# Performance work log

Measured on AMD Instinct MI355X. Metric: run time of the kernel, lower is better.

The kernel has to match this reference:

```python
import jax, jax.numpy as jnp
import numpy as np

N_NODES = 50000
N_EDGES = 800000
F_IN = 256
HID = 128
HEADS = 4
F_OUT = 64
NEG_SLOPE = 0.2


def setup_inputs() -> dict:
    key = jax.random.key(0)
    ks = jax.random.split(key, 12)
    x = jax.random.normal(ks[0], (N_NODES, F_IN), dtype=jnp.float32)
    edge_index = jax.random.randint(ks[1], (2, N_EDGES), 0, N_NODES, dtype=jnp.int64)
    s = 0.05
    return {
        "x": x,
        "edge_index": edge_index,
        "W1": jax.random.normal(ks[2], (F_IN, HEADS * HID), dtype=jnp.float32) * s,
        "a_src1": jax.random.normal(ks[3], (HEADS, HID), dtype=jnp.float32) * s,
        "a_dst1": jax.random.normal(ks[4], (HEADS, HID), dtype=jnp.float32) * s,
        "b1": jnp.zeros((HEADS * HID,), dtype=jnp.float32),
        "W2": jax.random.normal(ks[5], (HEADS * HID, F_OUT), dtype=jnp.float32) * s,
        "a_src2": jax.random.normal(ks[6], (1, F_OUT), dtype=jnp.float32) * s,
        "a_dst2": jax.random.normal(ks[7], (1, F_OUT), dtype=jnp.float32) * s,
        "b2": jnp.zeros((F_OUT,), dtype=jnp.float32),
    }


def _add_self_loops(edge_index, n):
    loop = jnp.arange(n, dtype=edge_index.dtype)
    return jnp.concatenate([edge_index, jnp.stack([loop, loop])], axis=1)


def _gat_conv(x, edge_index, W, a_src, a_dst, bias, heads, out_ch):
    # PyG GATConv: h = x @ W reshaped to [N, H, C]
    n = x.shape[0]
    h = (x @ W).reshape(n, heads, out_ch)
    # per-node attention logits [N, H]
    al_src = jnp.einsum('nhc,hc->nh', h, a_src)
    al_dst = jnp.einsum('nhc,hc->nh', h, a_dst)
    src, dst = edge_index[0], edge_index[1]
    e = jax.nn.leaky_relu(al_src[src] + al_dst[dst], NEG_SLOPE)  # [E, H]
    # softmax over incoming edges per destination node (segment softmax)
    e_max = jax.ops.segment_max(e, dst, num_segments=n)
    e_exp = jnp.exp(e - e_max[dst])
    denom = jax.ops.segment_sum(e_exp, dst, num_segments=n)
    alpha = e_exp / (denom[dst] + 1e-16)  # [E, H]
    msg = h[src] * alpha[:, :, None]  # [E, H, C]
    out = jax.ops.segment_sum(msg, dst, num_segments=n)  # [N, H, C]
    return out.reshape(n, heads * out_ch) + bias


def reference(x, edge_index, W1, a_src1, a_dst1, b1, W2, a_src2, a_dst2, b2):
    # Dropout layers are identity in eval mode.
    ei = _add_self_loops(edge_index, x.shape[0])
    h = jax.nn.elu(_gat_conv(x, ei, W1, a_src1, a_dst1, b1, HEADS, HID))
    out = _gat_conv(h, ei, W2, a_src2, a_dst2, b2, 1, F_OUT)
    return out
```

## Files before the change

kernel.cpp:

```cpp
#include <hip/hip_runtime.h>
#include <math.h>

#define N_NODES 50000
#define N_EDGES 800000
#define E_TOT   850000
#define F_IN    256
#define F1      512
#define HID     128
#define HEADS   4
#define F_OUT   64

typedef __attribute__((ext_vector_type(8))) short short8;
typedef __attribute__((ext_vector_type(4))) float f32x4;
typedef unsigned short ushort_t;
typedef unsigned int uint_t;

__device__ __forceinline__ float lrelu(float x){ return x > 0.f ? x : 0.2f*x; }
__device__ __forceinline__ float elu(float x){ return x > 0.f ? x : expm1f(x); }

__device__ __forceinline__ ushort_t f2b(float f){
  uint_t u = __builtin_bit_cast(uint_t, f);
  u += 0x7fffu + ((u >> 16) & 1u);
  return (ushort_t)(u >> 16);
}
__device__ __forceinline__ float blo(uint_t u){ return __builtin_bit_cast(float, u << 16); }
__device__ __forceinline__ float bhi(uint_t u){ return __builtin_bit_cast(float, u & 0xffff0000u); }
__device__ __forceinline__ float b2f(ushort_t s){ return __builtin_bit_cast(float, (uint_t)s << 16); }

__global__ void hist_kernel(const int* __restrict__ ei, int* __restrict__ deg){
  int e = blockIdx.x*blockDim.x + threadIdx.x;
  if (e >= E_TOT) return;
  int dst = (e < N_EDGES) ? ei[N_EDGES + e] : (e - N_EDGES);
  atomicAdd(&deg[dst], 1);
}

__global__ __launch_bounds__(256) void scan1_kernel(const int* __restrict__ deg,
                                                    int* __restrict__ offs,
                                                    int* __restrict__ bsum){
  __shared__ int sd[256];
  const int tid = threadIdx.x;
  const int i = blockIdx.x*256 + tid;
  int v = (i < N_NODES) ? deg[i] : 0;
  sd[tid] = v; __syncthreads();
  #pragma unroll
  for (int off = 1; off < 256; off <<= 1){
    int t = (tid >= off) ? sd[tid - off] : 0;
    __syncthreads();
    sd[tid] += t;
    __syncthreads();
  }
  if (i < N_NODES) offs[i] = sd[tid] - v;
  if (tid == 255) bsum[blockIdx.x] = sd[255];
}

__global__ __launch_bounds__(256) void scan2_kernel(const int* __restrict__ bsum,
                                                    int* __restrict__ bbase, int nb){
  __shared__ int sd[256];
  const int tid = threadIdx.x;
  int v = (tid < nb) ? bsum[tid] : 0;
  sd[tid] = v; __syncthreads();
  #pragma unroll
  for (int off = 1; off < 256; off <<= 1){
    int t = (tid >= off) ? sd[tid - off] : 0;
    __syncthreads();
    sd[tid] += t;
    __syncthreads();
  }
  if (tid < nb) bbase[tid] = sd[tid] - v;
}

__global__ __launch_bounds__(256) void scan3_kernel(int* __restrict__ offs,
                                                    const int* __restrict__ bbase,
                                                    int* __restrict__ cur){
  const int i = blockIdx.x*256 + threadIdx.x;
  if (i < N_NODES){
    int o = offs[i] + bbase[blockIdx.x];
    offs[i] = o;
    cur[i] = o;
  }
  if (blockIdx.x == 0 && threadIdx.x == 0) offs[N_NODES] = E_TOT;
}

__global__ void scatter_kernel(const int* __restrict__ ei, int* __restrict__ cur,
                               int* __restrict__ ssrc){
  int e = blockIdx.x*blockDim.x + threadIdx.x;
  if (e >= E_TOT) return;
  int src, dst;
  if (e < N_EDGES){ src = ei[e]; dst = ei[N_EDGES + e]; }
  else            { src = e - N_EDGES; dst = src; }
  int pos = atomicAdd(&cur[dst], 1);
  ssrc[pos] = src;
}

__global__ __launch_bounds__(256) void cvt_x_kernel(const float* __restrict__ x,
                                                    ushort_t* __restrict__ xb){
  const int t = blockIdx.x*256 + threadIdx.x;
  const float4 a = ((const float4*)x)[t*2];
  const float4 b = ((const float4*)x)[t*2 + 1];
  uint4 o;
  o.x = (uint_t)f2b(a.x) | ((uint_t)f2b(a.y) << 16);
  o.y = (uint_t)f2b(a.z) | ((uint_t)f2b(a.w) << 16);
  o.z = (uint_t)f2b(b.x) | ((uint_t)f2b(b.y) << 16);
  o.w = (uint_t)f2b(b.z) | ((uint_t)f2b(b.w) << 16);
  ((uint4*)xb)[t] = o;
}

__global__ __launch_bounds__(256) void transpose_bf16_kernel(const float* __restrict__ W,
                                                             ushort_t* __restrict__ Wt,
                                                             int K, int N){
  __shared__ float tile[64][65];
  const int k0 = blockIdx.x*64, n0 = blockIdx.y*64;
  const int c = threadIdx.x & 63, r4 = threadIdx.x >> 6;
  for (int r = r4; r < 64; r += 4)
    tile[r][c] = W[(size_t)(k0 + r)*N + n0 + c];
  __syncthreads();
  for (int r = r4; r < 64; r += 4)
    Wt[(size_t)(n0 + r)*K + k0 + c] = f2b(tile[c][r]);
}

template<int K, int WR, int WC>
__global__ __launch_bounds__(256) void gemm_bf16(const ushort_t* __restrict__ A,
                                                 const ushort_t* __restrict__ Bt,
                                                 ushort_t* __restrict__ C,
                                                 int M, int N){
  constexpr int BM = WR*64, BN = WC*64, BKP = 40;
  __shared__ ushort_t As[BM*BKP];
  __shared__ ushort_t Bs[BN*BKP];
  const int tid = threadIdx.x;
  const int wave = tid >> 6, lane = tid & 63, quad = lane >> 4, l16 = lane & 15;
  const int wm = wave % WR, wn = wave / WR;
  const int m0 = blockIdx.x*BM, n0 = blockIdx.y*BN;
  f32x4 acc[4][4] = {};
  for (int k0 = 0; k0 < K; k0 += 32){
    #pragma unroll
    for (int s = tid; s < BM*4; s += 256){
      int r = s >> 2, c = s & 3;
      int gr = m0 + r; if (gr >= M) gr = M - 1;
      *(uint4*)(As + r*BKP + c*8) = *(const uint4*)(A + (size_t)gr*K + k0 + c*8);
    }
    #pragma unroll
    for (int s = tid; s < BN*4; s += 256){
      int r = s >> 2, c = s & 3;
      *(uint4*)(Bs + r*BKP + c*8) = *(const uint4*)(Bt + (size_t)(n0 + r)*K + k0 + c*8);
    }
    __syncthreads();
    short8 af[4], bfr[4];
    #pragma unroll
    for (int i = 0; i < 4; ++i)
      af[i] = *(const short8*)(As + (wm*64 + i*16 + l16)*BKP + quad*8);
    #pragma unroll
    for (int j = 0; j < 4; ++j)
      bfr[j] = *(const short8*)(Bs + (wn*64 + j*16 + l16)*BKP + quad*8);
    #pragma unroll
    for (int i = 0; i < 4; ++i)
      #pragma unroll
      for (int j = 0; j < 4; ++j)
        acc[i][j] = __builtin_amdgcn_mfma_f32_16x16x32_bf16(af[i], bfr[j], acc[i][j], 0, 0, 0);
    __syncthreads();
  }
  #pragma unroll
  for (int i = 0; i < 4; ++i){
    #pragma unroll
    for (int r = 0; r < 4; ++r){
      int row = m0 + wm*64 + i*16 + quad*4 + r;
      if (row < M){
        #pragma unroll
        for (int j = 0; j < 4; ++j){
          int col = n0 + wn*64 + j*16 + l16;
          C[(size_t)row*N + col] = f2b(acc[i][j][r]);
        }
      }
    }
  }
}

__global__ __launch_bounds__(128) void logits1_kernel(const ushort_t* __restrict__ h1b,
                                                      const float* __restrict__ a_src,
                                                      const float* __restrict__ a_dst,
                                                      float* __restrict__ als,
                                                      float* __restrict__ ald){
  const int n = blockIdx.x;
  const int tid = threadIdx.x;
  const int head = tid >> 5, p = tid & 31;
  const uint2 v = *(const uint2*)(h1b + (size_t)n*F1 + tid*4);
  float h0 = blo(v.x), h1 = bhi(v.x), h2 = blo(v.y), h3 = bhi(v.y);
  const float4 as = *(const float4*)(a_src + head*HID + p*4);
  const float4 ad = *(const float4*)(a_dst + head*HID + p*4);
  float ds = h0*as.x + h1*as.y + h2*as.z + h3*as.w;
  float dd = h0*ad.x + h1*ad.y + h2*ad.z + h3*ad.w;
  #pragma unroll
  for (int off = 16; off >= 1; off >>= 1){
    ds += __shfl_down(ds, off, 32);
    dd += __shfl_down(dd, off, 32);
  }
  if (p == 0){ als[n*4 + head] = ds; ald[n*4 + head] = dd; }
}

__global__ __launch_bounds__(256) void agg1_kernel(const ushort_t* __restrict__ h1b,
                                                   const float* __restrict__ als,
                                                   const float* __restrict__ ald1,
                                                   const float* __restrict__ b1,
                                                   const int* __restrict__ offs,
                                                   const int* __restrict__ ssrc,
                                                   ushort_t* __restrict__ hb){
  __shared__ int   shsrc[4][64];
  __shared__ float shal[4][64][4];
  const int wave = threadIdx.x >> 6, lane = threadIdx.x & 63;
  const int n = blockIdx.x*4 + wave;
  const int head = lane >> 4;
  const float4 ald = ((const float4*)ald1)[n];
  const int s0 = offs[n], s1 = offs[n+1];

  float d0 = 0.f, d1 = 0.f, d2 = 0.f, d3 = 0.f;
  for (int e = s0 + lane; e < s1; e += 64){
    const int sc = ssrc[e];
    const float4 as = ((const float4*)als)[sc];
    d0 += __expf(lrelu(as.x + ald.x));
    d1 += __expf(lrelu(as.y + ald.y));
    d2 += __expf(lrelu(as.z + ald.z));
    d3 += __expf(lrelu(as.w + ald.w));
  }
  #pragma unroll
  for (int off = 32; off >= 1; off >>= 1){
    d0 += __shfl_xor(d0, off);
    d1 += __shfl_xor(d1, off);
    d2 += __shfl_xor(d2, off);
    d3 += __shfl_xor(d3, off);
  }
  const float den = (head == 0) ? d0 : (head == 1) ? d1 : (head == 2) ? d2 : d3;
  const float rd = 1.0f / (den + 1e-16f);

  float acc[8] = {0.f,0.f,0.f,0.f,0.f,0.f,0.f,0.f};
  for (int ce = s0; ce < s1; ce += 64){
    const int idx = ce + lane;
    if (idx < s1){
      const int sc = ssrc[idx];
      const float4 as = ((const float4*)als)[sc];
      shsrc[wave][lane] = sc;
      float4 a4;
      a4.x = __expf(lrelu(as.x + ald.x));
      a4.y = __expf(lrelu(as.y + ald.y));
      a4.z = __expf(lrelu(as.z + ald.z));
      a4.w = __expf(lrelu(as.w + ald.w));
      *(float4*)&shal[wave][lane][0] = a4;
    }
    const int nE = min(64, s1 - ce);
    for (int k = 0; k < nE; ++k){
      const int scb = shsrc[wave][k];
      const float al = shal[wave][k][head] * rd;
      const uint4 hv = *(const uint4*)(h1b + (size_t)scb*F1 + lane*8);
      acc[0] = fmaf(blo(hv.x), al, acc[0]);
      acc[1] = fmaf(bhi(hv.x), al, acc[1]);
      acc[2] = fmaf(blo(hv.y), al, acc[2]);
      acc[3] = fmaf(bhi(hv.y), al, acc[3]);
      acc[4] = fmaf(blo(hv.z), al, acc[4]);
      acc[5] = fmaf(bhi(hv.z), al, acc[5]);
      acc[6] = fmaf(blo(hv.w), al, acc[6]);
      acc[7] = fmaf(bhi(hv.w), al, acc[7]);
    }
  }
  const float4 ba = *(const float4*)(b1 + lane*8);
  const float4 bb = *(const float4*)(b1 + lane*8 + 4);
  float o0 = elu(acc[0] + ba.x), o1 = elu(acc[1] + ba.y);
  float o2 = elu(acc[2] + ba.z), o3 = elu(acc[3] + ba.w);
  float o4 = elu(acc[4] + bb.x), o5 = elu(acc[5] + bb.y);
  float o6 = elu(acc[6] + bb.z), o7 = elu(acc[7] + bb.w);
  uint4 o;
  o.x = (uint_t)f2b(o0) | ((uint_t)f2b(o1) << 16);
  o.y = (uint_t)f2b(o2) | ((uint_t)f2b(o3) << 16);
  o.z = (uint_t)f2b(o4) | ((uint_t)f2b(o5) << 16);
  o.w = (uint_t)f2b(o6) | ((uint_t)f2b(o7) << 16);
  *(uint4*)(hb + (size_t)n*F1 + lane*8) = o;
}

__global__ __launch_bounds__(64) void logits2_kernel(const ushort_t* __restrict__ gb,
                                                     const float* __restrict__ a_src,
                                                     const float* __restrict__ a_dst,
                                                     float* __restrict__ als,
                                                     float* __restrict__ ald){
  const int n = blockIdx.x;
  const int tid = threadIdx.x;
  const float v = b2f(gb[(size_t)n*F_OUT + tid]);
  float ds = v * a_src[tid];
  float dd = v * a_dst[tid];
  #pragma unroll
  for (int off = 32; off >= 1; off >>= 1){
    ds += __shfl_xor(ds, off);
    dd += __shfl_xor(dd, off);
  }
  if (tid == 0){ als[n] = ds; ald[n] = dd; }
}

__global__ __launch_bounds__(256) void agg2_kernel(const ushort_t* __restrict__ gb,
                                                   const float* __restrict__ als,
                                                   const float* __restrict__ ald2,
                                                   const float* __restrict__ b2,
                                                   const int* __restrict__ offs,
                                                   const int* __restrict__ ssrc,
                                                   float* __restrict__ out){
  __shared__ int   shsrc[4][64];
  __shared__ float shal[4][64];
  const int wave = threadIdx.x >> 6, lane = threadIdx.x & 63;
  const int n = blockIdx.x*4 + wave;
  const float ald = ald2[n];
  const int s0 = offs[n], s1 = offs[n+1];

  float dsum = 0.f;
  for (int e = s0 + lane; e < s1; e += 64)
    dsum += __expf(lrelu(als[ssrc[e]] + ald));
  #pragma unroll
  for (int off = 32; off >= 1; off >>= 1)
    dsum += __shfl_xor(dsum, off);
  const float rd = 1.0f / (dsum + 1e-16f);

  float acc = 0.f;
  for (int ce = s0; ce < s1; ce += 64){
    const int idx = ce + lane;
    if (idx < s1){
      const int sc = ssrc[idx];
      shsrc[wave][lane] = sc;
      shal[wave][lane] = __expf(lrelu(als[sc] + ald)) * rd;
    }
    const int nE = min(64, s1 - ce);
    for (int k = 0; k < nE; ++k){
      const int scb = shsrc[wave][k];
      const float al = shal[wave][k];
      acc = fmaf(b2f(gb[(size_t)scb*F_OUT + lane]), al, acc);
    }
  }
  out[(size_t)n*F_OUT + lane] = acc + b2[lane];
}

extern "C" void kernel_launch(void* const* d_in, const int* in_sizes, int n_in,
                              void* d_out, int out_size, void* d_ws, size_t ws_size,
                              hipStream_t stream){
  const float* x      = (const float*)d_in[0];
  const int*   ei     = (const int*)  d_in[1];
  const float* W1     = (const float*)d_in[2];
  const float* a_src1 = (const float*)d_in[3];
  const float* a_dst1 = (const float*)d_in[4];
  const float* b1     = (const float*)d_in[5];
  const float* W2     = (const float*)d_in[6];
  const float* a_src2 = (const float*)d_in[7];
  const float* a_dst2 = (const float*)d_in[8];
  const float* b2     = (const float*)d_in[9];
  float* out = (float*)d_out;

  char* ws = (char*)d_ws;
  ushort_t* h1b  = (ushort_t*)(ws + 0UL);
  ushort_t* hb   = (ushort_t*)(ws + 51200000UL);
  ushort_t* xb   = (ushort_t*)(ws + 102400000UL);
  ushort_t* gb   = (ushort_t*)(ws + 128000000UL);
  ushort_t* W1t  = (ushort_t*)(ws + 134400000UL);
  ushort_t* W2t  = (ushort_t*)(ws + 134662144UL);
  float*    als1 = (float*)   (ws + 134727680UL);
  float*    ald1 = (float*)   (ws + 135527680UL);
  float*    als2 = (float*)   (ws + 136327680UL);
  float*    ald2 = (float*)   (ws + 136527680UL);
  int*      deg  = (int*)     (ws + 136727680UL);
  int*      offs = (int*)     (ws + 136927680UL);
  int*      bsum = (int*)     (ws + 137127744UL);
  int*      bbase= (int*)     (ws + 137128544UL);
  int*      cur  = (int*)     (ws + 137129600UL);
  int*      ssrc = (int*)     (ws + 137329600UL);

  hipMemsetAsync(deg, 0, 200000, stream);

  const int eb = (E_TOT + 255) / 256;
  const int nb = (N_NODES + 255) / 256;
  hist_kernel   <<<eb, 256, 0, stream>>>(ei, deg);
  scan1_kernel  <<<nb, 256, 0, stream>>>(deg, offs, bsum);
  scan2_kernel  <<<1, 256, 0, stream>>>(bsum, bbase, nb);
  scan3_kernel  <<<nb, 256, 0, stream>>>(offs, bbase, cur);
  scatter_kernel<<<eb, 256, 0, stream>>>(ei, cur, ssrc);

  cvt_x_kernel        <<<6250, 256, 0, stream>>>(x, xb);
  transpose_bf16_kernel<<<dim3(4, 8), 256, 0, stream>>>(W1, W1t, F_IN, F1);
  transpose_bf16_kernel<<<dim3(8, 1), 256, 0, stream>>>(W2, W2t, F1, F_OUT);

  gemm_bf16<F_IN, 2, 2><<<dim3(391, 4), 256, 0, stream>>>(xb, W1t, h1b, N_NODES, F1);
  logits1_kernel<<<N_NODES, 128, 0, stream>>>(h1b, a_src1, a_dst1, als1, ald1);
  agg1_kernel   <<<12500, 256, 0, stream>>>(h1b, als1, ald1, b1, offs, ssrc, hb);

  gemm_bf16<F1, 4, 1><<<dim3(196, 1), 256, 0, stream>>>(hb, W2t, gb, N_NODES, F_OUT);
  logits2_kernel<<<N_NODES, 64, 0, stream>>>(gb, a_src2, a_dst2, als2, ald2);
  agg2_kernel   <<<12500, 256, 0, stream>>>(gb, als2, ald2, b2, offs, ssrc, out);
}
```

Baseline: 476.8 us.

## Add single-pass fast path for low-degree nodes with software-prefetched gathers

For nodes with at most 64 incoming edges, the aggregation kernels now compute attention weights once into shared memory. They accumulate the unnormalized weighted sum and the softmax denominator in the same loop, then normalize at the end, removing the separate denominator pass over edges. The gather loop is unrolled by four and prefetches the next four source rows to hide memory latency. Padded slots use source 0 with zero weight, which adds a few redundant loads.

```diff
diff --git a/kernel.cpp b/kernel.cpp
--- a/kernel.cpp
+++ b/kernel.cpp
@@ -196,6 +196,16 @@
   if (p == 0){ als[n*4 + head] = ds; ald[n*4 + head] = dd; }
 }
 
+#define FMA8(hv, al) do{ \
+  acc[0] = fmaf(blo((hv).x), (al), acc[0]); \
+  acc[1] = fmaf(bhi((hv).x), (al), acc[1]); \
+  acc[2] = fmaf(blo((hv).y), (al), acc[2]); \
+  acc[3] = fmaf(bhi((hv).y), (al), acc[3]); \
+  acc[4] = fmaf(blo((hv).z), (al), acc[4]); \
+  acc[5] = fmaf(bhi((hv).z), (al), acc[5]); \
+  acc[6] = fmaf(blo((hv).w), (al), acc[6]); \
+  acc[7] = fmaf(bhi((hv).w), (al), acc[7]); }while(0)
+
 __global__ __launch_bounds__(256) void agg1_kernel(const ushort_t* __restrict__ h1b,
                                                    const float* __restrict__ als,
                                                    const float* __restrict__ ald1,
@@ -210,6 +220,73 @@
   const int head = lane >> 4;
   const float4 ald = ((const float4*)ald1)[n];
   const int s0 = offs[n], s1 = offs[n+1];
+  const int nE = s1 - s0;
+
+  float acc[8] = {0.f,0.f,0.f,0.f,0.f,0.f,0.f,0.f};
+
+  if (nE <= 64){
+    float4 a4 = {0.f,0.f,0.f,0.f};
+    int sc = 0;
+    if (lane < nE){
+      sc = ssrc[s0 + lane];
+      const float4 as = ((const float4*)als)[sc];
+      a4.x = __expf(lrelu(as.x + ald.x));
+      a4.y = __expf(lrelu(as.y + ald.y));
+      a4.z = __expf(lrelu(as.z + ald.z));
+      a4.w = __expf(lrelu(as.w + ald.w));
+    }
+    shsrc[wave][lane] = sc;
+    *(float4*)&shal[wave][lane][0] = a4;
+
+    const ushort_t* hbase = h1b + lane*8;
+    const int nE4 = (nE + 3) & ~3;
+    float dsum = 0.f;
+
+    uint4 h0  = *(const uint4*)(hbase + ((size_t)shsrc[wave][0] << 9));
+    uint4 h1v = *(const uint4*)(hbase + ((size_t)shsrc[wave][1] << 9));
+    uint4 h2v = *(const uint4*)(hbase + ((size_t)shsrc[wave][2] << 9));
+    uint4 h3v = *(const uint4*)(hbase + ((size_t)shsrc[wave][3] << 9));
+    float al0 = shal[wave][0][head];
+    float al1 = shal[wave][1][head];
+    float al2 = shal[wave][2][head];
+    float al3 = shal[wave][3][head];
+    for (int k = 0; k < nE4; k += 4){
+      uint4 p0 = h0, p1 = h1v, p2 = h2v, p3 = h3v;
+      float q0 = 0.f, q1 = 0.f, q2 = 0.f, q3 = 0.f;
+      if (k + 4 < nE4){
+        p0 = *(const uint4*)(hbase + ((size_t)shsrc[wave][k+4] << 9));
+        p1 = *(const uint4*)(hbase + ((size_t)shsrc[wave][k+5] << 9));
+        p2 = *(const uint4*)(hbase + ((size_t)shsrc[wave][k+6] << 9));
+        p3 = *(const uint4*)(hbase + ((size_t)shsrc[wave][k+7] << 9));
+        q0 = shal[wave][k+4][head];
+        q1 = shal[wave][k+5][head];
+        q2 = shal[wave][k+6][head];
+        q3 = shal[wave][k+7][head];
+      }
+      dsum += (al0 + al1) + (al2 + al3);
+      FMA8(h0,  al0);
+      FMA8(h1v, al1);
+      FMA8(h2v, al2);
+      FMA8(h3v, al3);
+      h0 = p0; h1v = p1; h2v = p2; h3v = p3;
+      al0 = q0; al1 = q1; al2 = q2; al3 = q3;
+    }
+
+    const float rd = 1.0f / (dsum + 1e-16f);
+    const float4 ba = *(const float4*)(b1 + lane*8);
+    const float4 bb = *(const float4*)(b1 + lane*8 + 4);
+    float o0 = elu(fmaf(acc[0], rd, ba.x)), o1 = elu(fmaf(acc[1], rd, ba.y));
+    float o2 = elu(fmaf(acc[2], rd, ba.z)), o3 = elu(fmaf(acc[3], rd, ba.w));
+    float o4 = elu(fmaf(acc[4], rd, bb.x)), o5 = elu(fmaf(acc[5], rd, bb.y));
+    float o6 = elu(fmaf(acc[6], rd, bb.z)), o7 = elu(fmaf(acc[7], rd, bb.w));
+    uint4 o;
+    o.x = (uint_t)f2b(o0) | ((uint_t)f2b(o1) << 16);
+    o.y = (uint_t)f2b(o2) | ((uint_t)f2b(o3) << 16);
+    o.z = (uint_t)f2b(o4) | ((uint_t)f2b(o5) << 16);
+    o.w = (uint_t)f2b(o6) | ((uint_t)f2b(o7) << 16);
+    *(uint4*)(hb + (size_t)n*F1 + lane*8) = o;
+    return;
+  }
 
   float d0 = 0.f, d1 = 0.f, d2 = 0.f, d3 = 0.f;
   for (int e = s0 + lane; e < s1; e += 64){
@@ -230,7 +307,6 @@
   const float den = (head == 0) ? d0 : (head == 1) ? d1 : (head == 2) ? d2 : d3;
   const float rd = 1.0f / (den + 1e-16f);
 
-  float acc[8] = {0.f,0.f,0.f,0.f,0.f,0.f,0.f,0.f};
   for (int ce = s0; ce < s1; ce += 64){
     const int idx = ce + lane;
     if (idx < s1){
@@ -244,19 +320,12 @@
       a4.w = __expf(lrelu(as.w + ald.w));
       *(float4*)&shal[wave][lane][0] = a4;
     }
-    const int nE = min(64, s1 - ce);
-    for (int k = 0; k < nE; ++k){
+    const int nB = min(64, s1 - ce);
+    for (int k = 0; k < nB; ++k){
       const int scb = shsrc[wave][k];
       const float al = shal[wave][k][head] * rd;
       const uint4 hv = *(const uint4*)(h1b + (size_t)scb*F1 + lane*8);
-      acc[0] = fmaf(blo(hv.x), al, acc[0]);
-      acc[1] = fmaf(bhi(hv.x), al, acc[1]);
-      acc[2] = fmaf(blo(hv.y), al, acc[2]);
-      acc[3] = fmaf(bhi(hv.y), al, acc[3]);
-      acc[4] = fmaf(blo(hv.z), al, acc[4]);
-      acc[5] = fmaf(bhi(hv.z), al, acc[5]);
-      acc[6] = fmaf(blo(hv.w), al, acc[6]);
-      acc[7] = fmaf(bhi(hv.w), al, acc[7]);
+      FMA8(hv, al);
     }
   }
   const float4 ba = *(const float4*)(b1 + lane*8);
@@ -304,6 +373,54 @@
   const int n = blockIdx.x*4 + wave;
   const float ald = ald2[n];
   const int s0 = offs[n], s1 = offs[n+1];
+  const int nE = s1 - s0;
+
+  if (nE <= 64){
+    float av = 0.f; int sc = 0;
+    if (lane < nE){
+      sc = ssrc[s0 + lane];
+      av = __expf(lrelu(als[sc] + ald));
+    }
+    shsrc[wave][lane] = sc;
+    shal[wave][lane] = av;
+
+    const ushort_t* gbase = gb + lane;
+    const int nE4 = (nE + 3) & ~3;
+    float acc = 0.f, dsum = 0.f;
+
+    ushort_t v0 = gbase[(size_t)shsrc[wave][0] << 6];
+    ushort_t v1 = gbase[(size_t)shsrc[wave][1] << 6];
+    ushort_t v2 = gbase[(size_t)shsrc[wave][2] << 6];
+    ushort_t v3 = gbase[(size_t)shsrc[wave][3] << 6];
+    float al0 = shal[wave][0];
+    float al1 = shal[wave][1];
+    float al2 = shal[wave][2];
+    float al3 = shal[wave][3];
+    for (int k = 0; k < nE4; k += 4){
+      ushort_t p0 = v0, p1 = v1, p2 = v2, p3 = v3;
+      float q0 = 0.f, q1 = 0.f, q2 = 0.f, q3 = 0.f;
+      if (k + 4 < nE4){
+        p0 = gbase[(size_t)shsrc[wave][k+4] << 6];
+        p1 = gbase[(size_t)shsrc[wave][k+5] << 6];
+        p2 = gbase[(size_t)shsrc[wave][k+6] << 6];
+        p3 = gbase[(size_t)shsrc[wave][k+7] << 6];
+        q0 = shal[wave][k+4];
+        q1 = shal[wave][k+5];
+        q2 = shal[wave][k+6];
+        q3 = shal[wave][k+7];
+      }
+      dsum += (al0 + al1) + (al2 + al3);
+      acc = fmaf(b2f(v0), al0, acc);
+      acc = fmaf(b2f(v1), al1, acc);
+      acc = fmaf(b2f(v2), al2, acc);
+      acc = fmaf(b2f(v3), al3, acc);
+      v0 = p0; v1 = p1; v2 = p2; v3 = p3;
+      al0 = q0; al1 = q1; al2 = q2; al3 = q3;
+    }
+    const float rd = 1.0f / (dsum + 1e-16f);
+    out[(size_t)n*F_OUT + lane] = fmaf(acc, rd, b2[lane]);
+    return;
+  }
 
   float dsum = 0.f;
   for (int e = s0 + lane; e < s1; e += 64)
@@ -321,8 +438,8 @@
       shsrc[wave][lane] = sc;
       shal[wave][lane] = __expf(lrelu(als[sc] + ald)) * rd;
     }
-    const int nE = min(64, s1 - ce);
-    for (int k = 0; k < nE; ++k){
+    const int nB = min(64, s1 - ce);
+    for (int k = 0; k < nB; ++k){
       const int scb = shsrc[wave][k];
       const float al = shal[wave][k];
       acc = fmaf(b2f(gb[(size_t)scb*F_OUT + lane]), al, acc);
@@ -330,6 +447,8 @@
   }
   out[(size_t)n*F_OUT + lane] = acc + b2[lane];
 }
+
+#undef FMA8
 
 extern "C" void kernel_launch(void* const* d_in, const int* in_sizes, int n_in,
                               void* d_out, int out_size, void* d_ws, size_t ws_size,
```

Result: no change. 469.5 us, median of 2 (-1.5%).
